# Performance work log

Measured on AMD Instinct MI355X. Metric: run time of the kernel, lower is better.

## Reference

```python
import jax, jax.numpy as jnp
import numpy as np

N_NODES = 40000
N_EDGES = 640000
N_FEAT = 128
HIDDEN = 128
N_GRAPHS = 64


def _sage_conv(x, src, dst, Wl, b, Wr):
    # PyG SAGEConv (aggr='mean', root_weight=True, normalize=False):
    # out_i = W_l @ mean_{j in N(i)} x_j + b + W_r @ x_i
    msg = x[src]                                             # [E, F]
    s = jax.ops.segment_sum(msg, dst, num_segments=N_NODES)  # [N, F]
    deg = jax.ops.segment_sum(jnp.ones((src.shape[0],), x.dtype), dst,
                              num_segments=N_NODES)
    agg = s / jnp.maximum(deg, 1.0)[:, None]
    return agg @ Wl + b + x @ Wr


def setup_inputs() -> dict:
    key = jax.random.key(0)
    ks = jax.random.split(key, 12)
    sc = 1.0 / np.sqrt(N_FEAT)
    x = jax.random.normal(ks[0], (N_NODES, N_FEAT), dtype=jnp.float32)
    edge_index = jax.random.randint(ks[1], (2, N_EDGES), 0, N_NODES, dtype=jnp.int32)
    batch = jnp.sort(jax.random.randint(ks[2], (N_NODES,), 0, N_GRAPHS, dtype=jnp.int32))
    mk = lambda k, shp: (jax.random.normal(k, shp, dtype=jnp.float32) * sc)
    return {
        'x': x, 'edge_index': edge_index, 'batch': batch,
        'W1l': mk(ks[3], (N_FEAT, HIDDEN)), 'b1': jnp.zeros((HIDDEN,), jnp.float32),
        'W1r': mk(ks[4], (N_FEAT, HIDDEN)),
        'W2l': mk(ks[5], (HIDDEN, HIDDEN)), 'b2': jnp.zeros((HIDDEN,), jnp.float32),
        'W2r': mk(ks[6], (HIDDEN, HIDDEN)),
        'W3l': mk(ks[7], (HIDDEN, HIDDEN)), 'b3': jnp.zeros((HIDDEN,), jnp.float32),
        'W3r': mk(ks[8], (HIDDEN, HIDDEN)),
        'Wlin': mk(ks[9], (3 * HIDDEN, HIDDEN)), 'blin': jnp.zeros((HIDDEN,), jnp.float32),
    }


def reference(x, edge_index, batch, W1l, b1, W1r, W2l, b2, W2r, W3l, b3, W3r, Wlin, blin):
    src, dst = edge_index[0], edge_index[1]
    h1 = jax.nn.relu(_sage_conv(x, src, dst, W1l, b1, W1r))
    h2 = jax.nn.relu(_sage_conv(h1, src, dst, W2l, b2, W2r))
    h3 = jax.nn.relu(_sage_conv(h2, src, dst, W3l, b3, W3r))
    h = jnp.concatenate([h1, h2, h3], axis=1)                # [N, 3*H]
    pooled = jax.ops.segment_sum(h, batch, num_segments=N_GRAPHS)  # global_add_pool
    out = jax.nn.relu(pooled @ Wlin + blin)                  # [G, H]
    return out
```

## Files before the change

kernel.cpp:

```cpp
#include <hip/hip_runtime.h>
#include <hip/hip_bf16.h>

#define N_NODES 40000
#define N_EDGES 640000
#define NFEAT 128
#define NGRAPHS 64
#define ECAP 768

typedef __attribute__((ext_vector_type(8))) short short8;
typedef __attribute__((ext_vector_type(4))) float float4v;

static __device__ __forceinline__ float bf2f(unsigned short u) {
    unsigned int x = ((unsigned int)u) << 16;
    return __builtin_bit_cast(float, x);
}
static __device__ __forceinline__ unsigned short f2bf(float f) {
    unsigned int x = __builtin_bit_cast(unsigned int, f);
    unsigned int r = x + 0x7fffu + ((x >> 16) & 1u);
    return (unsigned short)(r >> 16);
}

__global__ void k_prep(const int* __restrict__ dst, int* __restrict__ deg,
                       const int* __restrict__ batch, int* __restrict__ goff,
                       const float* __restrict__ x, unsigned short* __restrict__ h0,
                       const float* __restrict__ Wl0, const float* __restrict__ Wr0,
                       const float* __restrict__ Wl1, const float* __restrict__ Wr1,
                       const float* __restrict__ Wl2, const float* __restrict__ Wr2,
                       unsigned short* __restrict__ Wt) {
    int b = blockIdx.x;
    if (b < 2500) {
        int e = b * 256 + threadIdx.x;
        if (e < N_EDGES) atomicAdd(&deg[dst[e]], 1);
    } else if (b < 2657) {
        int i = (b - 2500) * 256 + threadIdx.x;
        if (i >= N_NODES) return;
        int b1 = batch[i];
        int b0 = (i == 0) ? -1 : batch[i - 1];
        for (int g = b0 + 1; g <= b1; ++g) goff[g] = i;
        if (i == N_NODES - 1)
            for (int g = b1 + 1; g <= NGRAPHS; ++g) goff[g] = N_NODES;
    } else if (b < 12657) {
        int i = (b - 2657) * 256 + threadIdx.x;
        const int n = N_NODES * NFEAT / 2;
        if (i < n) {
            float a = x[2 * i], c = x[2 * i + 1];
            unsigned int u = (unsigned int)f2bf(a) | ((unsigned int)f2bf(c) << 16);
            ((unsigned int*)h0)[i] = u;
        }
    } else {
        int id = (b - 12657) * 256 + threadIdx.x;
        if (id >= 3 * 128 * 256) return;
        int l   = id >> 15;
        int rem = id & 32767;
        int nn  = rem >> 8;
        int k   = rem & 255;
        const float* Wl = (l == 0) ? Wl0 : (l == 1) ? Wl1 : Wl2;
        const float* Wr = (l == 0) ? Wr0 : (l == 1) ? Wr1 : Wr2;
        float v = (k < 128) ? Wl[k * 128 + nn] : Wr[(k - 128) * 128 + nn];
        Wt[id] = f2bf(v);
    }
}

__global__ __launch_bounds__(1024) void k_scan(const int* __restrict__ deg,
                                               int* __restrict__ offsets,
                                               int* __restrict__ cursor) {
    __shared__ int ws[16];
    __shared__ int s_boff;
    int tid = threadIdx.x;
    int b = blockIdx.x;
    int lane = tid & 63, wave = tid >> 6;

    int lim = b << 10;
    int s = 0;
    for (int i = tid; i < lim; i += 1024) s += deg[i];
    for (int d = 1; d < 64; d <<= 1) s += __shfl_xor(s, d, 64);
    if (lane == 0) ws[wave] = s;
    __syncthreads();
    if (tid == 0) {
        int t = 0;
        for (int w = 0; w < 16; ++w) t += ws[w];
        s_boff = t;
    }
    __syncthreads();
    int boff = s_boff;

    int i = (b << 10) + tid;
    int v = (i < N_NODES) ? deg[i] : 0;
    int incl = v;
    for (int d = 1; d < 64; d <<= 1) {
        int t = __shfl_up(incl, d, 64);
        if (lane >= d) incl += t;
    }
    __syncthreads();
    if (lane == 63) ws[wave] = incl;
    __syncthreads();
    if (wave == 0 && lane < 16) {
        int w = ws[lane];
        for (int d = 1; d < 16; d <<= 1) {
            int t = __shfl_up(w, d, 64);
            if (lane >= d) w += t;
        }
        ws[lane] = w;
    }
    __syncthreads();
    int waveOff = (wave == 0) ? 0 : ws[wave - 1];
    if (i < N_NODES) {
        int o = boff + waveOff + incl - v;
        offsets[i] = o;
        cursor[i]  = o;
    }
    if (b == 39 && tid == 0) offsets[N_NODES] = N_EDGES;
}

__global__ void k_fill(const int* __restrict__ src, const int* __restrict__ dst,
                       int* __restrict__ cursor, int* __restrict__ esrc) {
    int e = blockIdx.x * 256 + threadIdx.x;
    if (e < N_EDGES) {
        int d = dst[e];
        int p = atomicAdd(&cursor[d], 1);
        esrc[p] = src[e];
    }
}

__global__ __launch_bounds__(256, 8) void k_sage(
        const unsigned short* __restrict__ hin,
        const int* __restrict__ offsets,
        const int* __restrict__ esrc,
        const unsigned short* __restrict__ Wt,
        const float* __restrict__ bias,
        unsigned short* __restrict__ hout) {
    __shared__ __align__(16) unsigned short As[32][264];
    __shared__ int eidx[ECAP];
    int tid = threadIdx.x;
    int row0 = blockIdx.x * 32;

    int estart = offsets[row0];
    int ecnt   = offsets[row0 + 32] - estart;
    int staged = ecnt < ECAP ? ecnt : ECAP;

    for (int p = 0; p < 2; ++p) {
        int ci = tid + p * 256;
        int r = ci >> 4, c8 = ci & 15;
        uint4 v = *(const uint4*)(hin + (size_t)(row0 + r) * 128 + c8 * 8);
        *(uint4*)(&As[r][128 + c8 * 8]) = v;
    }
    for (int t = tid; t < staged; t += 256) eidx[t] = esrc[estart + t];
    __syncthreads();

    {
        int grp = tid >> 4;
        int sub = tid & 15;
        for (int nn = 0; nn < 2; ++nn) {
            int r = nn * 16 + grp;
            int node = row0 + r;
            int beg = offsets[node], end = offsets[node + 1];
            float a[8];
            for (int i = 0; i < 8; ++i) a[i] = 0.f;
            auto acc8 = [&](uint4 u) {
                a[0] += bf2f((unsigned short)(u.x & 0xffffu));
                a[1] += bf2f((unsigned short)(u.x >> 16));
                a[2] += bf2f((unsigned short)(u.y & 0xffffu));
                a[3] += bf2f((unsigned short)(u.y >> 16));
                a[4] += bf2f((unsigned short)(u.z & 0xffffu));
                a[5] += bf2f((unsigned short)(u.z >> 16));
                a[6] += bf2f((unsigned short)(u.w & 0xffffu));
                a[7] += bf2f((unsigned short)(u.w >> 16));
            };
            if (end - estart <= staged) {
                int lj = beg - estart, lend = end - estart;
                for (; lj + 8 <= lend; lj += 8) {
                    int s0 = eidx[lj],     s1 = eidx[lj + 1];
                    int s2 = eidx[lj + 2], s3 = eidx[lj + 3];
                    int s4 = eidx[lj + 4], s5 = eidx[lj + 5];
                    int s6 = eidx[lj + 6], s7 = eidx[lj + 7];
                    uint4 u0 = *(const uint4*)(hin + (size_t)s0 * 128 + sub * 8);
                    uint4 u1 = *(const uint4*)(hin + (size_t)s1 * 128 + sub * 8);
                    uint4 u2 = *(const uint4*)(hin + (size_t)s2 * 128 + sub * 8);
                    uint4 u3 = *(const uint4*)(hin + (size_t)s3 * 128 + sub * 8);
                    uint4 u4 = *(const uint4*)(hin + (size_t)s4 * 128 + sub * 8);
                    uint4 u5 = *(const uint4*)(hin + (size_t)s5 * 128 + sub * 8);
                    uint4 u6 = *(const uint4*)(hin + (size_t)s6 * 128 + sub * 8);
                    uint4 u7 = *(const uint4*)(hin + (size_t)s7 * 128 + sub * 8);
                    acc8(u0); acc8(u1); acc8(u2); acc8(u3);
                    acc8(u4); acc8(u5); acc8(u6); acc8(u7);
                }
                for (; lj < lend; ++lj) {
                    int s = eidx[lj];
                    uint4 u = *(const uint4*)(hin + (size_t)s * 128 + sub * 8);
                    acc8(u);
                }
            } else {
                for (int j = beg; j < end; ++j) {
                    int s = esrc[j];
                    uint4 u = *(const uint4*)(hin + (size_t)s * 128 + sub * 8);
                    acc8(u);
                }
            }
            int deg = end - beg;
            float inv = 1.f / (float)(deg > 1 ? deg : 1);
            uint4 v;
            v.x = (unsigned int)f2bf(a[0] * inv) | ((unsigned int)f2bf(a[1] * inv) << 16);
            v.y = (unsigned int)f2bf(a[2] * inv) | ((unsigned int)f2bf(a[3] * inv) << 16);
            v.z = (unsigned int)f2bf(a[4] * inv) | ((unsigned int)f2bf(a[5] * inv) << 16);
            v.w = (unsigned int)f2bf(a[6] * inv) | ((unsigned int)f2bf(a[7] * inv) << 16);
            *(uint4*)(&As[r][sub * 8]) = v;
        }
    }
    __syncthreads();

    int wave = tid >> 6, lane = tid & 63;
    int quad = lane >> 4, l16 = lane & 15;
    float4v acc[2][2];
    for (int rt = 0; rt < 2; ++rt)
        for (int ct = 0; ct < 2; ++ct) acc[rt][ct] = {0.f, 0.f, 0.f, 0.f};

    int ncol0 = wave * 32;
    for (int kc = 0; kc < 8; ++kc) {
        int k0 = kc * 32 + quad * 8;
        short8 a[2], b[2];
        for (int rt = 0; rt < 2; ++rt)
            a[rt] = *(const short8*)(&As[rt * 16 + l16][k0]);
        for (int ct = 0; ct < 2; ++ct)
            b[ct] = *(const short8*)(Wt + (size_t)(ncol0 + ct * 16 + l16) * 256 + k0);
        for (int rt = 0; rt < 2; ++rt)
            for (int ct = 0; ct < 2; ++ct)
                acc[rt][ct] = __builtin_amdgcn_mfma_f32_16x16x32_bf16(
                    a[rt], b[ct], acc[rt][ct], 0, 0, 0);
    }

    for (int ct = 0; ct < 2; ++ct) {
        int col = ncol0 + ct * 16 + l16;
        float bv = bias[col];
        for (int rt = 0; rt < 2; ++rt) {
            int r0 = rt * 16 + quad * 4;
            for (int i = 0; i < 4; ++i) {
                float v = acc[rt][ct][i] + bv;
                v = v > 0.f ? v : 0.f;
                hout[(size_t)(row0 + r0 + i) * 128 + col] = f2bf(v);
            }
        }
    }
}

__global__ __launch_bounds__(256) void k_pool(const unsigned short* __restrict__ h1,
                                              const unsigned short* __restrict__ h2,
                                              const unsigned short* __restrict__ h3,
                                              const int* __restrict__ goff,
                                              float* __restrict__ pooled) {
    __shared__ float red[4][16][8];
    int b = blockIdx.x;
    int g = b / 3, aidx = b % 3;
    const unsigned short* h = (aidx == 0) ? h1 : (aidx == 1) ? h2 : h3;
    int beg = goff[g], end = goff[g + 1];
    int tid = threadIdx.x;
    int rp = tid >> 4;
    int ch = tid & 15;
    float a[8];
    for (int i = 0; i < 8; ++i) a[i] = 0.f;
    for (int r = beg + rp; r < end; r += 16) {
        uint4 u = *(const uint4*)(h + (size_t)r * 128 + ch * 8);
        a[0] += bf2f((unsigned short)(u.x & 0xffffu));
        a[1] += bf2f((unsigned short)(u.x >> 16));
        a[2] += bf2f((unsigned short)(u.y & 0xffffu));
        a[3] += bf2f((unsigned short)(u.y >> 16));
        a[4] += bf2f((unsigned short)(u.z & 0xffffu));
        a[5] += bf2f((unsigned short)(u.z >> 16));
        a[6] += bf2f((unsigned short)(u.w & 0xffffu));
        a[7] += bf2f((unsigned short)(u.w >> 16));
    }
    for (int i = 0; i < 8; ++i) {
        a[i] += __shfl_xor(a[i], 16, 64);
        a[i] += __shfl_xor(a[i], 32, 64);
    }
    int wave = tid >> 6, lane = tid & 63;
    if (lane < 16)
        for (int i = 0; i < 8; ++i) red[wave][lane][i] = a[i];
    __syncthreads();
    if (tid < 128) {
        int ch2 = tid >> 3, e = tid & 7;
        float s = red[0][ch2][e] + red[1][ch2][e] + red[2][ch2][e] + red[3][ch2][e];
        pooled[g * 384 + aidx * 128 + ch2 * 8 + e] = s;
    }
}

__global__ void k_final(const float* __restrict__ pooled,
                        const float* __restrict__ Wlin,
                        const float* __restrict__ blin,
                        float* __restrict__ out) {
    int g = blockIdx.x, col = threadIdx.x;
    float acc = blin[col];
    for (int k = 0; k < 384; ++k)
        acc = fmaf(pooled[g * 384 + k], Wlin[k * 128 + col], acc);
    out[g * 128 + col] = acc > 0.f ? acc : 0.f;
}

extern "C" void kernel_launch(void* const* d_in, const int* in_sizes, int n_in,
                              void* d_out, int out_size, void* d_ws, size_t ws_size,
                              hipStream_t stream) {
    const float* x    = (const float*)d_in[0];
    const int*   ei   = (const int*)d_in[1];
    const int*   src  = ei;
    const int*   dst  = ei + N_EDGES;
    const int*   batch = (const int*)d_in[2];
    const float* W1l = (const float*)d_in[3];
    const float* b1  = (const float*)d_in[4];
    const float* W1r = (const float*)d_in[5];
    const float* W2l = (const float*)d_in[6];
    const float* b2  = (const float*)d_in[7];
    const float* W2r = (const float*)d_in[8];
    const float* W3l = (const float*)d_in[9];
    const float* b3  = (const float*)d_in[10];
    const float* W3r = (const float*)d_in[11];
    const float* Wlin = (const float*)d_in[12];
    const float* blin = (const float*)d_in[13];
    float* out = (float*)d_out;

    char* ws = (char*)d_ws;
    size_t off = 0;
    auto alloc = [&](size_t bytes) -> char* {
        char* p = ws + off;
        off = (off + bytes + 255) & ~(size_t)255;
        return p;
    };
    int* offsets = (int*)alloc((N_NODES + 1) * sizeof(int));
    int* cursor  = (int*)alloc(N_NODES * sizeof(int));
    int* deg     = (int*)alloc(N_NODES * sizeof(int));
    int* goff    = (int*)alloc((NGRAPHS + 1) * sizeof(int));
    int* esrc    = (int*)alloc(N_EDGES * sizeof(int));
    unsigned short* h0   = (unsigned short*)alloc((size_t)N_NODES * 128 * 2);
    unsigned short* h1   = (unsigned short*)alloc((size_t)N_NODES * 128 * 2);
    unsigned short* h2   = (unsigned short*)alloc((size_t)N_NODES * 128 * 2);
    unsigned short* h3   = (unsigned short*)alloc((size_t)N_NODES * 128 * 2);
    unsigned short* Wt   = (unsigned short*)alloc(3 * 256 * 128 * 2);
    float* pooled = (float*)alloc(NGRAPHS * 384 * sizeof(float));

    hipMemsetAsync(deg, 0, N_NODES * sizeof(int), stream);

    k_prep<<<13041, 256, 0, stream>>>(dst, deg, batch, goff, x, h0,
                                      W1l, W1r, W2l, W2r, W3l, W3r, Wt);
    k_scan<<<40, 1024, 0, stream>>>(deg, offsets, cursor);
    k_fill<<<(N_EDGES + 255) / 256, 256, 0, stream>>>(src, dst, cursor, esrc);

    k_sage<<<1250, 256, 0, stream>>>(h0, offsets, esrc, Wt,             b1, h1);
    k_sage<<<1250, 256, 0, stream>>>(h1, offsets, esrc, Wt + 32768,     b2, h2);
    k_sage<<<1250, 256, 0, stream>>>(h2, offsets, esrc, Wt + 2 * 32768, b3, h3);

    k_pool<<<3 * NGRAPHS, 256, 0, stream>>>(h1, h2, h3, goff, pooled);
    k_final<<<NGRAPHS, 128, 0, stream>>>(pooled, Wlin, blin, out);
}
```

Baseline: 275.7 us.

## Fuse global add pooling into SAGE epilogue and vectorize input conversion

Each SAGE layer's epilogue now stages its fp32 ReLU outputs in shared memory and does a segmented per-column reduction by graph id. It then atomically adds the partial sums into the pooled buffer, so the separate pooling kernel and the layer-3 output write are removed. The input x-to-bf16 conversion is vectorized to 8 elements per thread, and zeroing of the pooled buffer moves into the prep kernel. This adds an extra syncthreads, shared-memory traffic and global float atomics per block. Pooling now sums fp32 values instead of the bf16-rounded ones.

```diff
diff --git a/kernel.cpp b/kernel.cpp
--- a/kernel.cpp
+++ b/kernel.cpp
@@ -26,7 +26,7 @@
                        const float* __restrict__ Wl0, const float* __restrict__ Wr0,
                        const float* __restrict__ Wl1, const float* __restrict__ Wr1,
                        const float* __restrict__ Wl2, const float* __restrict__ Wr2,
-                       unsigned short* __restrict__ Wt) {
+                       unsigned short* __restrict__ Wt, float* __restrict__ pooled) {
     int b = blockIdx.x;
     if (b < 2500) {
         int e = b * 256 + threadIdx.x;
@@ -39,16 +39,21 @@
         for (int g = b0 + 1; g <= b1; ++g) goff[g] = i;
         if (i == N_NODES - 1)
             for (int g = b1 + 1; g <= NGRAPHS; ++g) goff[g] = N_NODES;
-    } else if (b < 12657) {
+    } else if (b < 5157) {
         int i = (b - 2657) * 256 + threadIdx.x;
-        const int n = N_NODES * NFEAT / 2;
+        const int n = N_NODES * NFEAT / 8;
         if (i < n) {
-            float a = x[2 * i], c = x[2 * i + 1];
-            unsigned int u = (unsigned int)f2bf(a) | ((unsigned int)f2bf(c) << 16);
-            ((unsigned int*)h0)[i] = u;
-        }
-    } else {
-        int id = (b - 12657) * 256 + threadIdx.x;
+            const float4* xf = (const float4*)x;
+            float4 p0 = xf[2 * i], p1 = xf[2 * i + 1];
+            uint4 v;
+            v.x = (unsigned int)f2bf(p0.x) | ((unsigned int)f2bf(p0.y) << 16);
+            v.y = (unsigned int)f2bf(p0.z) | ((unsigned int)f2bf(p0.w) << 16);
+            v.z = (unsigned int)f2bf(p1.x) | ((unsigned int)f2bf(p1.y) << 16);
+            v.w = (unsigned int)f2bf(p1.z) | ((unsigned int)f2bf(p1.w) << 16);
+            ((uint4*)h0)[i] = v;
+        }
+    } else if (b < 5541) {
+        int id = (b - 5157) * 256 + threadIdx.x;
         if (id >= 3 * 128 * 256) return;
         int l   = id >> 15;
         int rem = id & 32767;
@@ -58,6 +63,9 @@
         const float* Wr = (l == 0) ? Wr0 : (l == 1) ? Wr1 : Wr2;
         float v = (k < 128) ? Wl[k * 128 + nn] : Wr[(k - 128) * 128 + nn];
         Wt[id] = f2bf(v);
+    } else {
+        int j = (b - 5541) * 256 + threadIdx.x;
+        if (j < NGRAPHS * 384) pooled[j] = 0.f;
     }
 }
 
@@ -126,9 +134,11 @@
         const unsigned short* __restrict__ hin,
         const int* __restrict__ offsets,
         const int* __restrict__ esrc,
+        const int* __restrict__ batch,
         const unsigned short* __restrict__ Wt,
         const float* __restrict__ bias,
-        unsigned short* __restrict__ hout) {
+        unsigned short* __restrict__ hout,
+        float* __restrict__ poolseg) {
     __shared__ __align__(16) unsigned short As[32][264];
     __shared__ int eidx[ECAP];
     int tid = threadIdx.x;
@@ -228,6 +238,11 @@
                     a[rt], b[ct], acc[rt][ct], 0, 0, 0);
     }
 
+    __syncthreads();
+    float* Ps = (float*)&As[0][0];
+    int* sbatch = eidx;
+    if (tid < 32) sbatch[tid] = batch[row0 + tid];
+
     for (int ct = 0; ct < 2; ++ct) {
         int col = ncol0 + ct * 16 + l16;
         float bv = bias[col];
@@ -236,50 +251,29 @@
             for (int i = 0; i < 4; ++i) {
                 float v = acc[rt][ct][i] + bv;
                 v = v > 0.f ? v : 0.f;
-                hout[(size_t)(row0 + r0 + i) * 128 + col] = f2bf(v);
+                if (hout) hout[(size_t)(row0 + r0 + i) * 128 + col] = f2bf(v);
+                Ps[(r0 + i) * 132 + col] = v;
             }
         }
     }
-}
-
-__global__ __launch_bounds__(256) void k_pool(const unsigned short* __restrict__ h1,
-                                              const unsigned short* __restrict__ h2,
-                                              const unsigned short* __restrict__ h3,
-                                              const int* __restrict__ goff,
-                                              float* __restrict__ pooled) {
-    __shared__ float red[4][16][8];
-    int b = blockIdx.x;
-    int g = b / 3, aidx = b % 3;
-    const unsigned short* h = (aidx == 0) ? h1 : (aidx == 1) ? h2 : h3;
-    int beg = goff[g], end = goff[g + 1];
-    int tid = threadIdx.x;
-    int rp = tid >> 4;
-    int ch = tid & 15;
-    float a[8];
-    for (int i = 0; i < 8; ++i) a[i] = 0.f;
-    for (int r = beg + rp; r < end; r += 16) {
-        uint4 u = *(const uint4*)(h + (size_t)r * 128 + ch * 8);
-        a[0] += bf2f((unsigned short)(u.x & 0xffffu));
-        a[1] += bf2f((unsigned short)(u.x >> 16));
-        a[2] += bf2f((unsigned short)(u.y & 0xffffu));
-        a[3] += bf2f((unsigned short)(u.y >> 16));
-        a[4] += bf2f((unsigned short)(u.z & 0xffffu));
-        a[5] += bf2f((unsigned short)(u.z >> 16));
-        a[6] += bf2f((unsigned short)(u.w & 0xffffu));
-        a[7] += bf2f((unsigned short)(u.w >> 16));
-    }
-    for (int i = 0; i < 8; ++i) {
-        a[i] += __shfl_xor(a[i], 16, 64);
-        a[i] += __shfl_xor(a[i], 32, 64);
-    }
-    int wave = tid >> 6, lane = tid & 63;
-    if (lane < 16)
-        for (int i = 0; i < 8; ++i) red[wave][lane][i] = a[i];
-    __syncthreads();
-    if (tid < 128) {
-        int ch2 = tid >> 3, e = tid & 7;
-        float s = red[0][ch2][e] + red[1][ch2][e] + red[2][ch2][e] + red[3][ch2][e];
-        pooled[g * 384 + aidx * 128 + ch2 * 8 + e] = s;
+    __syncthreads();
+
+    {
+        int half = tid >> 7;
+        int c = tid & 127;
+        int rbase = half * 16;
+        float accp = 0.f;
+        int cur = sbatch[rbase];
+        for (int r = rbase; r < rbase + 16; ++r) {
+            int g = sbatch[r];
+            if (g != cur) {
+                atomicAdd(&poolseg[cur * 384 + c], accp);
+                accp = 0.f;
+                cur = g;
+            }
+            accp += Ps[r * 132 + c];
+        }
+        atomicAdd(&poolseg[cur * 384 + c], accp);
     }
 }
 
@@ -330,21 +324,22 @@
     unsigned short* h0   = (unsigned short*)alloc((size_t)N_NODES * 128 * 2);
     unsigned short* h1   = (unsigned short*)alloc((size_t)N_NODES * 128 * 2);
     unsigned short* h2   = (unsigned short*)alloc((size_t)N_NODES * 128 * 2);
-    unsigned short* h3   = (unsigned short*)alloc((size_t)N_NODES * 128 * 2);
     unsigned short* Wt   = (unsigned short*)alloc(3 * 256 * 128 * 2);
     float* pooled = (float*)alloc(NGRAPHS * 384 * sizeof(float));
 
     hipMemsetAsync(deg, 0, N_NODES * sizeof(int), stream);
 
-    k_prep<<<13041, 256, 0, stream>>>(dst, deg, batch, goff, x, h0,
-                                      W1l, W1r, W2l, W2r, W3l, W3r, Wt);
+    k_prep<<<5637, 256, 0, stream>>>(dst, deg, batch, goff, x, h0,
+                                     W1l, W1r, W2l, W2r, W3l, W3r, Wt, pooled);
     k_scan<<<40, 1024, 0, stream>>>(deg, offsets, cursor);
     k_fill<<<(N_EDGES + 255) / 256, 256, 0, stream>>>(src, dst, cursor, esrc);
 
-    k_sage<<<1250, 256, 0, stream>>>(h0, offsets, esrc, Wt,             b1, h1);
-    k_sage<<<1250, 256, 0, stream>>>(h1, offsets, esrc, Wt + 32768,     b2, h2);
-    k_sage<<<1250, 256, 0, stream>>>(h2, offsets, esrc, Wt + 2 * 32768, b3, h3);
-
-    k_pool<<<3 * NGRAPHS, 256, 0, stream>>>(h1, h2, h3, goff, pooled);
+    k_sage<<<1250, 256, 0, stream>>>(h0, offsets, esrc, batch, Wt,
+                                     b1, h1, pooled);
+    k_sage<<<1250, 256, 0, stream>>>(h1, offsets, esrc, batch, Wt + 32768,
+                                     b2, h2, pooled + 128);
+    k_sage<<<1250, 256, 0, stream>>>(h2, offsets, esrc, batch, Wt + 2 * 32768,
+                                     b3, (unsigned short*)nullptr, pooled + 256);
+
     k_final<<<NGRAPHS, 128, 0, stream>>>(pooled, Wlin, blin, out);
 }
```

Result: faster. 263.7 us (-4.4%).
